# Performance work log

Hardware: AMD Instinct MI355X
Metric: run time of the kernel (lower is better)

## Reference

```python
import jax, jax.numpy as jnp
import numpy as np

SEQ_LEN = 2048

def setup_inputs() -> dict:
    key = jax.random.key(0)
    k1, k2, k3 = jax.random.split(key, 3)
    B, H, S, D = 4, 16, SEQ_LEN, 64
    keys_t = jax.random.normal(k1, (B, H, S, D), dtype=jnp.float32)
    queries = jax.random.normal(k2, (B, H, S, D), dtype=jnp.float32)
    values = jax.random.normal(k3, (B, H, S, D), dtype=jnp.float32)
    return {"keys": keys_t, "queries": queries, "values": values, "head_dim": D}

def reference(keys, queries, values, head_dim):
    # scores: [B, H, S, S] = Q K^T / sqrt(d)
    scale = 1.0 / jnp.sqrt(jnp.float32(head_dim))
    scores = jnp.einsum('bhqd,bhkd->bhqk', queries, keys) * scale
    S = scores.shape[-1]
    # causal mask: positions where tril == 0 (k > q) get -inf
    causal = jnp.tril(jnp.ones((S, S), dtype=bool))
    scores = jnp.where(causal, scores, -jnp.inf)
    attn = jax.nn.softmax(scores, axis=-1)
    # dropout p=0.0 -> identity
    return jnp.einsum('bhqk,bhkd->bhqd', attn, values)
```

## Files before the change

kernel.cpp:

```cpp
#include <hip/hip_runtime.h>
#include <hip/hip_bf16.h>

typedef __bf16 bf16x8 __attribute__((ext_vector_type(8)));
typedef __bf16 bf16x4 __attribute__((ext_vector_type(4)));
typedef float  f32x4  __attribute__((ext_vector_type(4)));

#define S_LEN 2048
#define DH    64
#define QB    64
#define KVB   64
#define NT    (S_LEN / KVB)
#define TILE_ELEMS 8192
#define TILE_BYTES 16384
#define L2E   1.44269504088896f

__device__ __forceinline__ int swz(int row, int col) {
    return (row << 6) + ((((col >> 3) ^ row) & 7) << 3) + (col & 7);
}

__device__ __forceinline__ void gl2lds16(const void* g, void* l) {
    __builtin_amdgcn_global_load_lds(
        (const __attribute__((address_space(1))) void*)g,
        (__attribute__((address_space(3))) void*)l, 16, 0, 0);
}

__device__ __forceinline__ float fexp2(float x) {
    return __builtin_amdgcn_exp2f(x);
}

__launch_bounds__(256, 4)
__global__ void prep_kv(const float* __restrict__ Kg,
                        const float* __restrict__ Vg,
                        __bf16* __restrict__ blob) {
    __shared__ __bf16 Vtmp[64 * 72];
    const int bt  = blockIdx.x;
    const int tid = threadIdx.x;
    const size_t gbase = (size_t)bt * (KVB * DH);
    const float* Kt = Kg + gbase;
    const float* Vt = Vg + gbase;
    __bf16* outK = blob + (size_t)bt * TILE_ELEMS;
    __bf16* outV = outK + 4096;

    #pragma unroll
    for (int u = 0; u < 2; ++u) {
        const int m   = tid * 2 + u;
        const int row = m >> 3, cc = m & 7;
        const int c   = cc ^ (row & 7);
        const float* src = Kt + row * DH + c * 8;
        f32x4 a = *(const f32x4*)src;
        f32x4 b = *(const f32x4*)(src + 4);
        bf16x8 o;
        #pragma unroll
        for (int j = 0; j < 4; ++j) { o[j] = (__bf16)a[j]; o[j + 4] = (__bf16)b[j]; }
        *(bf16x8*)&outK[m * 8] = o;
    }
    {
        const int kv = tid >> 2, dq = (tid & 3) * 16;
        const float* src = Vt + kv * DH + dq;
        f32x4 v0 = *(const f32x4*)src,        v1 = *(const f32x4*)(src + 4);
        f32x4 v2 = *(const f32x4*)(src + 8),  v3 = *(const f32x4*)(src + 12);
        bf16x8 o0, o1;
        #pragma unroll
        for (int j = 0; j < 4; ++j) {
            o0[j] = (__bf16)v0[j]; o0[j + 4] = (__bf16)v1[j];
            o1[j] = (__bf16)v2[j]; o1[j + 4] = (__bf16)v3[j];
        }
        *(bf16x8*)&Vtmp[kv * 72 + dq]     = o0;
        *(bf16x8*)&Vtmp[kv * 72 + dq + 8] = o1;
    }
    __syncthreads();
    #pragma unroll
    for (int u = 0; u < 2; ++u) {
        const int m  = tid * 2 + u;
        const int d  = m >> 3, cc = m & 7;
        const int S8 = cc ^ (d & 7);
        const int kc = S8 >> 2, hs = S8 & 3;
        bf16x8 o;
        #pragma unroll
        for (int j = 0; j < 8; ++j) {
            const int kv = (kc * 2 + (j >> 2)) * 16 + hs * 4 + (j & 3);
            o[j] = Vtmp[kv * 72 + d];
        }
        *(bf16x8*)&outV[m * 8] = o;
    }
}

__launch_bounds__(256, 4)
__global__ void attn_seq(const float* __restrict__ Qg,
                         float* __restrict__ Og,
                         const __bf16* __restrict__ blob) {
    __shared__ __bf16 Klds[2][4096];
    __shared__ __bf16 Vlds[2][4096];

    const int f   = blockIdx.x;
    const int chn = gridDim.x >> 3;
    const int fs  = (f & 7) * chn + (f >> 3);
    const int bh  = fs >> 4;
    const int p   = fs & 15;
    const int qa  = p;
    const int qbg = NT - 1 - p;

    const int tid = threadIdx.x;
    const int w   = tid >> 6;
    const int l   = tid & 63;
    const int lo  = l & 15;
    const int hi  = l >> 4;

    const size_t base = (size_t)bh * S_LEN * DH;
    const float* Qb = Qg + base;
    float*       Ob = Og + base;
    const char*  blobB = (const char*)(blob + (size_t)bh * NT * TILE_ELEMS);

    int koff[4][2];
    #pragma unroll
    for (int c = 0; c < 4; ++c) {
        koff[c][0] = swz(c * 16 + lo, hi * 8);
        koff[c][1] = swz(c * 16 + lo, 32 + hi * 8);
    }

    bf16x8 bq0, bq1, bqB0, bqB1;
    {
        const float* pa = Qb + (size_t)(qa  * QB + w * 16 + lo) * DH + hi * 8;
        const float* pb = Qb + (size_t)(qbg * QB + w * 16 + lo) * DH + hi * 8;
        f32x4 a0 = *(const f32x4*)pa,        a1 = *(const f32x4*)(pa + 4);
        f32x4 a2 = *(const f32x4*)(pa + 32), a3 = *(const f32x4*)(pa + 36);
        f32x4 b0 = *(const f32x4*)pb,        b1 = *(const f32x4*)(pb + 4);
        f32x4 b2 = *(const f32x4*)(pb + 32), b3 = *(const f32x4*)(pb + 36);
        #pragma unroll
        for (int j = 0; j < 4; ++j) {
            bq0[j]  = (__bf16)(a0[j] * 0.125f); bq0[j + 4]  = (__bf16)(a1[j] * 0.125f);
            bq1[j]  = (__bf16)(a2[j] * 0.125f); bq1[j + 4]  = (__bf16)(a3[j] * 0.125f);
            bqB0[j] = (__bf16)(b0[j] * 0.125f); bqB0[j + 4] = (__bf16)(b1[j] * 0.125f);
            bqB1[j] = (__bf16)(b2[j] * 0.125f); bqB1[j + 4] = (__bf16)(b3[j] * 0.125f);
        }
    }

    f32x4 oacc[4];
    #pragma unroll
    for (int n = 0; n < 4; ++n) oacc[n] = (f32x4){0.f, 0.f, 0.f, 0.f};
    float mrow = -1e30f, lrow = 0.f;

    auto stage = [&](int buf, int t) {
        const char* tb = blobB + (size_t)t * TILE_BYTES;
        char* kd = (char*)&Klds[buf][w * 1024];
        char* vd = (char*)&Vlds[buf][w * 1024];
        const char* ks = tb + w * 2048 + l * 16;
        const char* vs = tb + 8192 + w * 2048 + l * 16;
        gl2lds16(ks,        kd);
        gl2lds16(ks + 1024, kd + 1024);
        gl2lds16(vs,        vd);
        gl2lds16(vs + 1024, vd + 1024);
    };

    auto writeO = [&](int qt) {
        const float linv = 1.0f / lrow;
        const int   q    = qt * QB + w * 16 + lo;
        #pragma unroll
        for (int n = 0; n < 4; ++n) {
            f32x4 o;
            #pragma unroll
            for (int r = 0; r < 4; ++r) o[r] = oacc[n][r] * linv;
            *(f32x4*)(Ob + (size_t)q * DH + n * 16 + hi * 4) = o;
        }
    };

    stage(0, 0);
    __syncthreads();

    for (int u = 0; u <= 32; ++u) {
        const int cur = u & 1;
        if (u < 32) {
            const int tn = (u + 1 <= qa) ? (u + 1) : (u - qa);
            stage(cur ^ 1, tn);
        }
        const bool diag = (u == qa) || (u == 32);
        const __bf16* Kc = &Klds[cur][0];
        const __bf16* Vc = &Vlds[cur][0];

        f32x4 sc[4];
        __builtin_amdgcn_s_setprio(1);
        #pragma unroll
        for (int c = 0; c < 4; ++c) {
            bf16x8 ak0 = *(const bf16x8*)&Kc[koff[c][0]];
            bf16x8 ak1 = *(const bf16x8*)&Kc[koff[c][1]];
            f32x4 acc = (f32x4){0.f, 0.f, 0.f, 0.f};
            acc = __builtin_amdgcn_mfma_f32_16x16x32_bf16(ak0, bq0, acc, 0, 0, 0);
            acc = __builtin_amdgcn_mfma_f32_16x16x32_bf16(ak1, bq1, acc, 0, 0, 0);
            sc[c] = acc;
        }
        __builtin_amdgcn_s_setprio(0);

        if (diag) {
            const int qloc = w * 16 + lo;
            #pragma unroll
            for (int c = 0; c < 4; ++c)
                #pragma unroll
                for (int r = 0; r < 4; ++r)
                    if (c * 16 + hi * 4 + r > qloc) sc[c][r] = -1e30f;
        }

        float pm = -1e30f;
        #pragma unroll
        for (int c = 0; c < 4; ++c)
            pm = fmaxf(pm, fmaxf(fmaxf(sc[c][0], sc[c][1]),
                                 fmaxf(sc[c][2], sc[c][3])));
        pm = fmaxf(pm, __shfl_xor(pm, 16, 64));
        pm = fmaxf(pm, __shfl_xor(pm, 32, 64));

        if (!__all(pm - mrow <= 5.545f)) {
            const float mn = fmaxf(mrow, pm);
            const float fr = fexp2((mrow - mn) * L2E);
            mrow = mn; lrow *= fr;
            #pragma unroll
            for (int n = 0; n < 4; ++n) oacc[n] *= fr;
        }
        const float mL = mrow * L2E;
        float rs = 0.f;
        #pragma unroll
        for (int c = 0; c < 4; ++c)
            #pragma unroll
            for (int r = 0; r < 4; ++r) {
                float pe = fexp2(fmaf(sc[c][r], L2E, -mL));
                sc[c][r] = pe;
                rs += pe;
            }
        rs += __shfl_xor(rs, 16, 64);
        rs += __shfl_xor(rs, 32, 64);
        lrow += rs;

        bf16x8 pb[2];
        #pragma unroll
        for (int kc = 0; kc < 2; ++kc)
            #pragma unroll
            for (int j = 0; j < 8; ++j)
                pb[kc][j] = (__bf16)sc[kc * 2 + (j >> 2)][j & 3];

        __builtin_amdgcn_s_setprio(1);
        #pragma unroll
        for (int n = 0; n < 4; ++n) {
            bf16x8 av0 = *(const bf16x8*)&Vc[koff[n][0]];
            bf16x8 av1 = *(const bf16x8*)&Vc[koff[n][1]];
            oacc[n] = __builtin_amdgcn_mfma_f32_16x16x32_bf16(av0, pb[0], oacc[n], 0, 0, 0);
            oacc[n] = __builtin_amdgcn_mfma_f32_16x16x32_bf16(av1, pb[1], oacc[n], 0, 0, 0);
        }
        __builtin_amdgcn_s_setprio(0);

        __syncthreads();

        if (u == qa) {
            writeO(qa);
            #pragma unroll
            for (int n = 0; n < 4; ++n) oacc[n] = (f32x4){0.f, 0.f, 0.f, 0.f};
            mrow = -1e30f; lrow = 0.f;
            bq0 = bqB0; bq1 = bqB1;
        }
    }

    writeO(qbg);
}

__launch_bounds__(256, 4)
__global__ void attn_fwd(const float* __restrict__ Kg,
                         const float* __restrict__ Qg,
                         const float* __restrict__ Vg,
                         float* __restrict__ Og) {
    __shared__ __bf16 Klds[64 * 64];
    __shared__ __bf16 Vlds[64 * 64];

    const int qb  = blockIdx.x;
    const int bh  = blockIdx.y;
    const int tid = threadIdx.x;
    const int w   = tid >> 6;
    const int l   = tid & 63;
    const int lo  = l & 15;
    const int hi  = l >> 4;

    const int    q0   = qb * QB;
    const size_t base = (size_t)bh * S_LEN * DH;
    const float* Kb = Kg + base;
    const float* Qb = Qg + base;
    const float* Vb = Vg + base;
    float*       Ob = Og + base;

    bf16x8 bq[2];
    {
        const int qrow = q0 + w * 16 + lo;
        #pragma unroll
        for (int dc = 0; dc < 2; ++dc) {
            const float* p = Qb + (size_t)qrow * DH + dc * 32 + hi * 8;
            f32x4 v0 = *(const f32x4*)p;
            f32x4 v1 = *(const f32x4*)(p + 4);
            #pragma unroll
            for (int j = 0; j < 4; ++j) {
                bq[dc][j]     = (__bf16)(v0[j] * 0.125f);
                bq[dc][j + 4] = (__bf16)(v1[j] * 0.125f);
            }
        }
    }

    f32x4 oacc[4];
    #pragma unroll
    for (int n = 0; n < 4; ++n) oacc[n] = (f32x4){0.f, 0.f, 0.f, 0.f};
    float mrow = -1e30f, lrow = 0.f;

    const int krr = tid >> 4;
    const int kc4 = (tid & 15) * 4;

    for (int t = 0; t <= qb; ++t) {
        const int kv0 = t * KVB;
        {
            const float* kp = Kb + (size_t)kv0 * DH + kc4;
            #pragma unroll
            for (int i = 0; i < 4; ++i) {
                const int row = i * 16 + krr;
                f32x4 k4 = *(const f32x4*)(kp + (size_t)row * DH);
                bf16x4 kb;
                #pragma unroll
                for (int j = 0; j < 4; ++j) kb[j] = (__bf16)k4[j];
                *(bf16x4*)&Klds[swz(row, kc4)] = kb;
            }
        }
        {
            const float* vp = Vb + (size_t)kv0 * DH + l;
            float vv[16];
            #pragma unroll
            for (int i = 0; i < 16; ++i) {
                const int s  = w * 16 + i;
                const int kc = s >> 5, hs = (s >> 3) & 3, j = s & 7;
                const int kv = (kc * 2 + (j >> 2)) * 16 + hs * 4 + (j & 3);
                vv[i] = vp[(size_t)kv * DH];
            }
            bf16x8 v0, v1;
            #pragma unroll
            for (int i = 0; i < 8; ++i) { v0[i] = (__bf16)vv[i]; v1[i] = (__bf16)vv[8 + i]; }
            *(bf16x8*)&Vlds[swz(l, w * 16)]     = v0;
            *(bf16x8*)&Vlds[swz(l, w * 16 + 8)] = v1;
        }
        __syncthreads();

        const bool diag = (t == qb);
        const int  cmax = diag ? (w + 1) : 4;
        f32x4 sc[4];
        #pragma unroll
        for (int c = 0; c < 4; ++c) {
            if (c < cmax) {
                f32x4 acc = (f32x4){0.f, 0.f, 0.f, 0.f};
                #pragma unroll
                for (int dc = 0; dc < 2; ++dc) {
                    bf16x8 ak = *(const bf16x8*)&Klds[swz(c * 16 + lo, dc * 32 + hi * 8)];
                    acc = __builtin_amdgcn_mfma_f32_16x16x32_bf16(ak, bq[dc], acc, 0, 0, 0);
                }
                sc[c] = acc;
            } else {
                sc[c] = (f32x4){-1e30f, -1e30f, -1e30f, -1e30f};
            }
        }
        if (diag) {
            #pragma unroll
            for (int r = 0; r < 4; ++r)
                if (hi * 4 + r > lo) sc[w][r] = -1e30f;
        }

        float pm = -1e30f;
        #pragma unroll
        for (int c = 0; c < 4; ++c)
            #pragma unroll
            for (int r = 0; r < 4; ++r) pm = fmaxf(pm, sc[c][r]);
        pm = fmaxf(pm, __shfl_xor(pm, 16, 64));
        pm = fmaxf(pm, __shfl_xor(pm, 32, 64));

        const float mn = fmaxf(mrow, pm);
        const float fr = __expf(mrow - mn);
        mrow = mn;
        float rs = 0.f;
        #pragma unroll
        for (int c = 0; c < 4; ++c)
            #pragma unroll
            for (int r = 0; r < 4; ++r) {
                float pe = __expf(sc[c][r] - mn);
                sc[c][r] = pe;
                rs += pe;
            }
        rs += __shfl_xor(rs, 16, 64);
        rs += __shfl_xor(rs, 32, 64);
        lrow = lrow * fr + rs;
        #pragma unroll
        for (int n = 0; n < 4; ++n) oacc[n] *= fr;

        bf16x8 pb[2];
        #pragma unroll
        for (int kc = 0; kc < 2; ++kc)
            #pragma unroll
            for (int j = 0; j < 8; ++j)
                pb[kc][j] = (__bf16)sc[kc * 2 + (j >> 2)][j & 3];

        #pragma unroll
        for (int n = 0; n < 4; ++n) {
            #pragma unroll
            for (int kc = 0; kc < 2; ++kc) {
                bf16x8 av = *(const bf16x8*)&Vlds[swz(n * 16 + lo, kc * 32 + hi * 8)];
                oacc[n] = __builtin_amdgcn_mfma_f32_16x16x32_bf16(av, pb[kc], oacc[n], 0, 0, 0);
            }
        }
        __syncthreads();
    }

    const float linv = 1.0f / lrow;
    const int   q    = q0 + w * 16 + lo;
    #pragma unroll
    for (int n = 0; n < 4; ++n) {
        f32x4 o;
        #pragma unroll
        for (int r = 0; r < 4; ++r) o[r] = oacc[n][r] * linv;
        *(f32x4*)(Ob + (size_t)q * DH + n * 16 + hi * 4) = o;
    }
}

extern "C" void kernel_launch(void* const* d_in, const int* in_sizes, int n_in,
                              void* d_out, int out_size, void* d_ws, size_t ws_size,
                              hipStream_t stream) {
    const float* keys    = (const float*)d_in[0];
    const float* queries = (const float*)d_in[1];
    const float* values  = (const float*)d_in[2];
    float* out = (float*)d_out;

    const int    BH   = in_sizes[0] / (S_LEN * DH);
    const size_t need = (size_t)BH * NT * TILE_BYTES;
    const int    nblk = (NT / 2) * BH;

    if (ws_size >= need && (nblk % 8) == 0) {
        prep_kv<<<dim3(BH * NT), 256, 0, stream>>>(keys, values, (__bf16*)d_ws);
        attn_seq<<<dim3(nblk), 256, 0, stream>>>(queries, out,
                                                 (const __bf16*)d_ws);
    } else {
        attn_fwd<<<dim3(S_LEN / QB, BH), 256, 0, stream>>>(keys, queries, values, out);
    }
}
```

Before: 83.34 us.

## Split long causal query blocks across two KV halves and merge partial outputs

Adds a new attention kernel where each 128-thread block handles a 64-row query tile with two 16-row groups per wave. Query tiles in the upper half of the sequence are split into two KV-range parts whose partial output, max and sum are written to workspace, and a separate merge kernel combines them. Lower-half tiles are processed whole. The aim is to balance causal work across blocks and give each wave more MFMA reuse of K/V fragments. It also adds a lazy rescale that skips the output rescale when the running max grows by at most a small threshold. In exchange it pays an extra kernel launch, workspace traffic for the partials, and uses half-size blocks. The old fallback kernel is removed, so nothing runs if workspace is too small.

```diff
diff --git a/kernel.cpp b/kernel.cpp
--- a/kernel.cpp
+++ b/kernel.cpp
@@ -12,6 +12,7 @@
 #define NT    (S_LEN / KVB)
 #define TILE_ELEMS 8192
 #define TILE_BYTES 16384
+#define PSLOT 4224
 #define L2E   1.44269504088896f
 
 __device__ __forceinline__ int swz(int row, int col) {
@@ -85,6 +86,239 @@
     }
 }
 
+__launch_bounds__(128, 2)
+__global__ void attn_sp(const float* __restrict__ Qg,
+                        float* __restrict__ Og,
+                        const __bf16* __restrict__ blob,
+                        float* __restrict__ partials) {
+    __shared__ __bf16 Klds[2][4096];
+    __shared__ __bf16 Vlds[2][4096];
+
+    const int bh = blockIdx.x;
+    const int j  = blockIdx.y;
+    int qb, part, t0, len;
+    if (j < 32) {
+        qb   = 31 - (j >> 1);
+        part = j & 1;
+        const int h = (qb + 2) >> 1;
+        t0  = part ? h : 0;
+        len = part ? (qb + 1 - h) : h;
+    } else {
+        qb   = 47 - j;
+        part = 2;
+        t0   = 0;
+        len  = qb + 1;
+    }
+    const bool hasDiag = (part != 0);
+    const int  diagIt  = hasDiag ? len - 1 : -1;
+
+    const int tid = threadIdx.x;
+    const int w   = tid >> 6;
+    const int l   = tid & 63;
+    const int lo  = l & 15;
+    const int hi  = l >> 4;
+
+    const size_t base = (size_t)bh * S_LEN * DH;
+    const float* Qb = Qg + base;
+    float*       Ob = Og + base;
+    const char*  blobB = (const char*)(blob + (size_t)bh * NT * TILE_ELEMS);
+
+    int koff[4][2];
+    #pragma unroll
+    for (int c = 0; c < 4; ++c) {
+        koff[c][0] = swz(c * 16 + lo, hi * 8);
+        koff[c][1] = swz(c * 16 + lo, 32 + hi * 8);
+    }
+
+    bf16x8 bq[2][2];
+    #pragma unroll
+    for (int g = 0; g < 2; ++g) {
+        const float* pq = Qb + (size_t)(qb * QB + w * 32 + g * 16 + lo) * DH + hi * 8;
+        f32x4 a0 = *(const f32x4*)pq,        a1 = *(const f32x4*)(pq + 4);
+        f32x4 a2 = *(const f32x4*)(pq + 32), a3 = *(const f32x4*)(pq + 36);
+        #pragma unroll
+        for (int jj = 0; jj < 4; ++jj) {
+            bq[g][0][jj]     = (__bf16)(a0[jj] * 0.125f);
+            bq[g][0][jj + 4] = (__bf16)(a1[jj] * 0.125f);
+            bq[g][1][jj]     = (__bf16)(a2[jj] * 0.125f);
+            bq[g][1][jj + 4] = (__bf16)(a3[jj] * 0.125f);
+        }
+    }
+
+    f32x4 oacc[2][4];
+    #pragma unroll
+    for (int g = 0; g < 2; ++g)
+        #pragma unroll
+        for (int n = 0; n < 4; ++n) oacc[g][n] = (f32x4){0.f, 0.f, 0.f, 0.f};
+    float mrow[2] = {-1e30f, -1e30f}, lrow[2] = {0.f, 0.f};
+
+    auto stage = [&](int buf, int t) {
+        const char* tb = blobB + (size_t)t * TILE_BYTES;
+        char* kd = (char*)&Klds[buf][0] + w * 4096;
+        char* vd = (char*)&Vlds[buf][0] + w * 4096;
+        const char* ks = tb + w * 4096 + l * 16;
+        const char* vs = tb + 8192 + w * 4096 + l * 16;
+        #pragma unroll
+        for (int i = 0; i < 4; ++i) {
+            gl2lds16(ks + i * 1024, kd + i * 1024);
+            gl2lds16(vs + i * 1024, vd + i * 1024);
+        }
+    };
+
+    stage(0, t0);
+    __syncthreads();
+
+    for (int it = 0; it < len; ++it) {
+        const int cur = it & 1;
+        if (it + 1 < len) stage(cur ^ 1, t0 + it + 1);
+        const bool diag = (it == diagIt);
+        const __bf16* Kc = &Klds[cur][0];
+        const __bf16* Vc = &Vlds[cur][0];
+
+        f32x4 sc[2][4];
+        __builtin_amdgcn_s_setprio(1);
+        #pragma unroll
+        for (int c = 0; c < 4; ++c) {
+            bf16x8 ak0 = *(const bf16x8*)&Kc[koff[c][0]];
+            bf16x8 ak1 = *(const bf16x8*)&Kc[koff[c][1]];
+            #pragma unroll
+            for (int g = 0; g < 2; ++g) {
+                f32x4 acc = (f32x4){0.f, 0.f, 0.f, 0.f};
+                acc = __builtin_amdgcn_mfma_f32_16x16x32_bf16(ak0, bq[g][0], acc, 0, 0, 0);
+                acc = __builtin_amdgcn_mfma_f32_16x16x32_bf16(ak1, bq[g][1], acc, 0, 0, 0);
+                sc[g][c] = acc;
+            }
+        }
+        __builtin_amdgcn_s_setprio(0);
+
+        if (diag) {
+            #pragma unroll
+            for (int g = 0; g < 2; ++g) {
+                const int qloc = w * 32 + g * 16 + lo;
+                #pragma unroll
+                for (int c = 0; c < 4; ++c)
+                    #pragma unroll
+                    for (int r = 0; r < 4; ++r)
+                        if (c * 16 + hi * 4 + r > qloc) sc[g][c][r] = -1e30f;
+            }
+        }
+
+        bf16x8 pb[2][2];
+        #pragma unroll
+        for (int g = 0; g < 2; ++g) {
+            float pm = -1e30f;
+            #pragma unroll
+            for (int c = 0; c < 4; ++c)
+                pm = fmaxf(pm, fmaxf(fmaxf(sc[g][c][0], sc[g][c][1]),
+                                     fmaxf(sc[g][c][2], sc[g][c][3])));
+            pm = fmaxf(pm, __shfl_xor(pm, 16, 64));
+            pm = fmaxf(pm, __shfl_xor(pm, 32, 64));
+            if (!__all(pm - mrow[g] <= 5.545f)) {
+                const float mn = fmaxf(mrow[g], pm);
+                const float fr = fexp2((mrow[g] - mn) * L2E);
+                mrow[g] = mn; lrow[g] *= fr;
+                #pragma unroll
+                for (int n = 0; n < 4; ++n) oacc[g][n] *= fr;
+            }
+            const float mL = mrow[g] * L2E;
+            float rs = 0.f;
+            #pragma unroll
+            for (int c = 0; c < 4; ++c)
+                #pragma unroll
+                for (int r = 0; r < 4; ++r) {
+                    float pe = fexp2(fmaf(sc[g][c][r], L2E, -mL));
+                    sc[g][c][r] = pe;
+                    rs += pe;
+                }
+            rs += __shfl_xor(rs, 16, 64);
+            rs += __shfl_xor(rs, 32, 64);
+            lrow[g] += rs;
+            #pragma unroll
+            for (int kc = 0; kc < 2; ++kc)
+                #pragma unroll
+                for (int jj = 0; jj < 8; ++jj)
+                    pb[g][kc][jj] = (__bf16)sc[g][kc * 2 + (jj >> 2)][jj & 3];
+        }
+
+        __builtin_amdgcn_s_setprio(1);
+        #pragma unroll
+        for (int n = 0; n < 4; ++n) {
+            bf16x8 av0 = *(const bf16x8*)&Vc[koff[n][0]];
+            bf16x8 av1 = *(const bf16x8*)&Vc[koff[n][1]];
+            #pragma unroll
+            for (int g = 0; g < 2; ++g) {
+                oacc[g][n] = __builtin_amdgcn_mfma_f32_16x16x32_bf16(av0, pb[g][0], oacc[g][n], 0, 0, 0);
+                oacc[g][n] = __builtin_amdgcn_mfma_f32_16x16x32_bf16(av1, pb[g][1], oacc[g][n], 0, 0, 0);
+            }
+        }
+        __builtin_amdgcn_s_setprio(0);
+
+        __syncthreads();
+    }
+
+    if (part == 2) {
+        #pragma unroll
+        for (int g = 0; g < 2; ++g) {
+            const float linv = 1.0f / lrow[g];
+            const int   q    = qb * QB + w * 32 + g * 16 + lo;
+            #pragma unroll
+            for (int n = 0; n < 4; ++n) {
+                f32x4 o;
+                #pragma unroll
+                for (int r = 0; r < 4; ++r) o[r] = oacc[g][n][r] * linv;
+                *(f32x4*)(Ob + (size_t)q * DH + n * 16 + hi * 4) = o;
+            }
+        }
+    } else {
+        const int pi = bh * 16 + (qb - 16);
+        float* fb = partials + (size_t)pi * 2 * PSLOT + part * PSLOT;
+        #pragma unroll
+        for (int g = 0; g < 2; ++g) {
+            const int row = w * 32 + g * 16 + lo;
+            #pragma unroll
+            for (int n = 0; n < 4; ++n)
+                *(f32x4*)&fb[row * 64 + n * 16 + hi * 4] = oacc[g][n];
+            if (hi == 0) {
+                fb[4096 + row] = mrow[g];
+                fb[4160 + row] = lrow[g];
+            }
+        }
+    }
+}
+
+__launch_bounds__(256, 4)
+__global__ void attn_merge(float* __restrict__ Og,
+                           const float* __restrict__ partials) {
+    const int bh = blockIdx.x;
+    const int y  = blockIdx.y;
+    const int qb = 16 + y;
+    const int pi = bh * 16 + y;
+    const float* s0 = partials + (size_t)pi * 2 * PSLOT;
+    const float* s1 = s0 + PSLOT;
+
+    const int tid = threadIdx.x;
+    const int row = tid >> 2;
+    const int cb  = (tid & 3) * 16;
+
+    const float m0 = s0[4096 + row], l0 = s0[4160 + row];
+    const float m1 = s1[4096 + row], l1 = s1[4160 + row];
+    const float M  = fmaxf(m0, m1);
+    const float w0 = fexp2((m0 - M) * L2E);
+    const float w1 = fexp2((m1 - M) * L2E);
+    const float inv = 1.0f / (w0 * l0 + w1 * l1);
+
+    float* out = Og + ((size_t)bh * S_LEN + qb * QB + row) * DH + cb;
+    #pragma unroll
+    for (int i = 0; i < 4; ++i) {
+        f32x4 a = *(const f32x4*)&s0[row * 64 + cb + i * 4];
+        f32x4 b = *(const f32x4*)&s1[row * 64 + cb + i * 4];
+        f32x4 o;
+        #pragma unroll
+        for (int r = 0; r < 4; ++r) o[r] = (w0 * a[r] + w1 * b[r]) * inv;
+        *(f32x4*)&out[i * 4] = o;
+    }
+}
+
 __launch_bounds__(256, 4)
 __global__ void attn_seq(const float* __restrict__ Qg,
                          float* __restrict__ Og,
@@ -127,11 +361,11 @@
         f32x4 b0 = *(const f32x4*)pb,        b1 = *(const f32x4*)(pb + 4);
         f32x4 b2 = *(const f32x4*)(pb + 32), b3 = *(const f32x4*)(pb + 36);
         #pragma unroll
-        for (int j = 0; j < 4; ++j) {
-            bq0[j]  = (__bf16)(a0[j] * 0.125f); bq0[j + 4]  = (__bf16)(a1[j] * 0.125f);
-            bq1[j]  = (__bf16)(a2[j] * 0.125f); bq1[j + 4]  = (__bf16)(a3[j] * 0.125f);
-            bqB0[j] = (__bf16)(b0[j] * 0.125f); bqB0[j + 4] = (__bf16)(b1[j] * 0.125f);
-            bqB1[j] = (__bf16)(b2[j] * 0.125f); bqB1[j + 4] = (__bf16)(b3[j] * 0.125f);
+        for (int jj = 0; jj < 4; ++jj) {
+            bq0[jj]  = (__bf16)(a0[jj] * 0.125f); bq0[jj + 4]  = (__bf16)(a1[jj] * 0.125f);
+            bq1[jj]  = (__bf16)(a2[jj] * 0.125f); bq1[jj + 4]  = (__bf16)(a3[jj] * 0.125f);
+            bqB0[jj] = (__bf16)(b0[jj] * 0.125f); bqB0[jj + 4] = (__bf16)(b1[jj] * 0.125f);
+            bqB1[jj] = (__bf16)(b2[jj] * 0.125f); bqB1[jj + 4] = (__bf16)(b3[jj] * 0.125f);
         }
     }
 
@@ -232,8 +466,8 @@
         #pragma unroll
         for (int kc = 0; kc < 2; ++kc)
             #pragma unroll
-            for (int j = 0; j < 8; ++j)
-                pb[kc][j] = (__bf16)sc[kc * 2 + (j >> 2)][j & 3];
+            for (int jj = 0; jj < 8; ++jj)
+                pb[kc][jj] = (__bf16)sc[kc * 2 + (jj >> 2)][jj & 3];
 
         __builtin_amdgcn_s_setprio(1);
         #pragma unroll
@@ -257,163 +491,6 @@
     }
 
     writeO(qbg);
-}
-
-__launch_bounds__(256, 4)
-__global__ void attn_fwd(const float* __restrict__ Kg,
-                         const float* __restrict__ Qg,
-                         const float* __restrict__ Vg,
-                         float* __restrict__ Og) {
-    __shared__ __bf16 Klds[64 * 64];
-    __shared__ __bf16 Vlds[64 * 64];
-
-    const int qb  = blockIdx.x;
-    const int bh  = blockIdx.y;
-    const int tid = threadIdx.x;
-    const int w   = tid >> 6;
-    const int l   = tid & 63;
-    const int lo  = l & 15;
-    const int hi  = l >> 4;
-
-    const int    q0   = qb * QB;
-    const size_t base = (size_t)bh * S_LEN * DH;
-    const float* Kb = Kg + base;
-    const float* Qb = Qg + base;
-    const float* Vb = Vg + base;
-    float*       Ob = Og + base;
-
-    bf16x8 bq[2];
-    {
-        const int qrow = q0 + w * 16 + lo;
-        #pragma unroll
-        for (int dc = 0; dc < 2; ++dc) {
-            const float* p = Qb + (size_t)qrow * DH + dc * 32 + hi * 8;
-            f32x4 v0 = *(const f32x4*)p;
-            f32x4 v1 = *(const f32x4*)(p + 4);
-            #pragma unroll
-            for (int j = 0; j < 4; ++j) {
-                bq[dc][j]     = (__bf16)(v0[j] * 0.125f);
-                bq[dc][j + 4] = (__bf16)(v1[j] * 0.125f);
-            }
-        }
-    }
-
-    f32x4 oacc[4];
-    #pragma unroll
-    for (int n = 0; n < 4; ++n) oacc[n] = (f32x4){0.f, 0.f, 0.f, 0.f};
-    float mrow = -1e30f, lrow = 0.f;
-
-    const int krr = tid >> 4;
-    const int kc4 = (tid & 15) * 4;
-
-    for (int t = 0; t <= qb; ++t) {
-        const int kv0 = t * KVB;
-        {
-            const float* kp = Kb + (size_t)kv0 * DH + kc4;
-            #pragma unroll
-            for (int i = 0; i < 4; ++i) {
-                const int row = i * 16 + krr;
-                f32x4 k4 = *(const f32x4*)(kp + (size_t)row * DH);
-                bf16x4 kb;
-                #pragma unroll
-                for (int j = 0; j < 4; ++j) kb[j] = (__bf16)k4[j];
-                *(bf16x4*)&Klds[swz(row, kc4)] = kb;
-            }
-        }
-        {
-            const float* vp = Vb + (size_t)kv0 * DH + l;
-            float vv[16];
-            #pragma unroll
-            for (int i = 0; i < 16; ++i) {
-                const int s  = w * 16 + i;
-                const int kc = s >> 5, hs = (s >> 3) & 3, j = s & 7;
-                const int kv = (kc * 2 + (j >> 2)) * 16 + hs * 4 + (j & 3);
-                vv[i] = vp[(size_t)kv * DH];
-            }
-            bf16x8 v0, v1;
-            #pragma unroll
-            for (int i = 0; i < 8; ++i) { v0[i] = (__bf16)vv[i]; v1[i] = (__bf16)vv[8 + i]; }
-            *(bf16x8*)&Vlds[swz(l, w * 16)]     = v0;
-            *(bf16x8*)&Vlds[swz(l, w * 16 + 8)] = v1;
-        }
-        __syncthreads();
-
-        const bool diag = (t == qb);
-        const int  cmax = diag ? (w + 1) : 4;
-        f32x4 sc[4];
-        #pragma unroll
-        for (int c = 0; c < 4; ++c) {
-            if (c < cmax) {
-                f32x4 acc = (f32x4){0.f, 0.f, 0.f, 0.f};
-                #pragma unroll
-                for (int dc = 0; dc < 2; ++dc) {
-                    bf16x8 ak = *(const bf16x8*)&Klds[swz(c * 16 + lo, dc * 32 + hi * 8)];
-                    acc = __builtin_amdgcn_mfma_f32_16x16x32_bf16(ak, bq[dc], acc, 0, 0, 0);
-                }
-                sc[c] = acc;
-            } else {
-                sc[c] = (f32x4){-1e30f, -1e30f, -1e30f, -1e30f};
-            }
-        }
-        if (diag) {
-            #pragma unroll
-            for (int r = 0; r < 4; ++r)
-                if (hi * 4 + r > lo) sc[w][r] = -1e30f;
-        }
-
-        float pm = -1e30f;
-        #pragma unroll
-        for (int c = 0; c < 4; ++c)
-            #pragma unroll
-            for (int r = 0; r < 4; ++r) pm = fmaxf(pm, sc[c][r]);
-        pm = fmaxf(pm, __shfl_xor(pm, 16, 64));
-        pm = fmaxf(pm, __shfl_xor(pm, 32, 64));
-
-        const float mn = fmaxf(mrow, pm);
-        const float fr = __expf(mrow - mn);
-        mrow = mn;
-        float rs = 0.f;
-        #pragma unroll
-        for (int c = 0; c < 4; ++c)
-            #pragma unroll
-            for (int r = 0; r < 4; ++r) {
-                float pe = __expf(sc[c][r] - mn);
-                sc[c][r] = pe;
-                rs += pe;
-            }
-        rs += __shfl_xor(rs, 16, 64);
-        rs += __shfl_xor(rs, 32, 64);
-        lrow = lrow * fr + rs;
-        #pragma unroll
-        for (int n = 0; n < 4; ++n) oacc[n] *= fr;
-
-        bf16x8 pb[2];
-        #pragma unroll
-        for (int kc = 0; kc < 2; ++kc)
-            #pragma unroll
-            for (int j = 0; j < 8; ++j)
-                pb[kc][j] = (__bf16)sc[kc * 2 + (j >> 2)][j & 3];
-
-        #pragma unroll
-        for (int n = 0; n < 4; ++n) {
-            #pragma unroll
-            for (int kc = 0; kc < 2; ++kc) {
-                bf16x8 av = *(const bf16x8*)&Vlds[swz(n * 16 + lo, kc * 32 + hi * 8)];
-                oacc[n] = __builtin_amdgcn_mfma_f32_16x16x32_bf16(av, pb[kc], oacc[n], 0, 0, 0);
-            }
-        }
-        __syncthreads();
-    }
-
-    const float linv = 1.0f / lrow;
-    const int   q    = q0 + w * 16 + lo;
-    #pragma unroll
-    for (int n = 0; n < 4; ++n) {
-        f32x4 o;
-        #pragma unroll
-        for (int r = 0; r < 4; ++r) o[r] = oacc[n][r] * linv;
-        *(f32x4*)(Ob + (size_t)q * DH + n * 16 + hi * 4) = o;
-    }
 }
 
 extern "C" void kernel_launch(void* const* d_in, const int* in_sizes, int n_in,
@@ -424,15 +501,20 @@
     const float* values  = (const float*)d_in[2];
     float* out = (float*)d_out;
 
-    const int    BH   = in_sizes[0] / (S_LEN * DH);
-    const size_t need = (size_t)BH * NT * TILE_BYTES;
-    const int    nblk = (NT / 2) * BH;
-
-    if (ws_size >= need && (nblk % 8) == 0) {
+    const int    BH        = in_sizes[0] / (S_LEN * DH);
+    const size_t blob_b    = (size_t)BH * NT * TILE_BYTES;
+    const size_t part_b    = (size_t)BH * 16 * 2 * PSLOT * 4;
+    const int    nblk      = (NT / 2) * BH;
+
+    if (ws_size >= blob_b + part_b && BH == 64) {
+        float* partials = (float*)((char*)d_ws + blob_b);
+        prep_kv<<<dim3(BH * NT), 256, 0, stream>>>(keys, values, (__bf16*)d_ws);
+        attn_sp<<<dim3(BH, 48), 128, 0, stream>>>(queries, out,
+                                                  (const __bf16*)d_ws, partials);
+        attn_merge<<<dim3(BH, 16), 256, 0, stream>>>(out, partials);
+    } else if (ws_size >= blob_b && (nblk % 8) == 0) {
         prep_kv<<<dim3(BH * NT), 256, 0, stream>>>(keys, values, (__bf16*)d_ws);
         attn_seq<<<dim3(nblk), 256, 0, stream>>>(queries, out,
                                                  (const __bf16*)d_ws);
-    } else {
-        attn_fwd<<<dim3(S_LEN / QB, BH), 256, 0, stream>>>(keys, queries, values, out);
-    }
-}
+    }
+}
```

Result: slower. 104.1 us (+24.9%).

## Split KV work across two blocks per query-tile pair with partial-result merge

Applied to the files above, without the earlier changes.

Adds a kernel that processes 32-row KV subtiles and splits each pair of causal query tiles across two blocks. One block does the short tile plus part of the long tile, the other does the rest, and each writes bf16 partial outputs with row max and sum. A small merge kernel combines the two partials for the upper query tiles. The aim is to double grid parallelism and balance work per block at higher occupancy, at the cost of an extra launch, partial-output traffic and bf16 rounding of the partials. The old fallback kernel is removed.

```diff
diff --git a/kernel.cpp b/kernel.cpp
--- a/kernel.cpp
+++ b/kernel.cpp
@@ -85,6 +85,239 @@
     }
 }
 
+__launch_bounds__(256, 8)
+__global__ void attn32(const float* __restrict__ Qg,
+                       float* __restrict__ Og,
+                       const __bf16* __restrict__ blob,
+                       __bf16* __restrict__ Opart,
+                       float* __restrict__ mlpart) {
+    __shared__ __bf16 Klds[2][2048];
+    __shared__ __bf16 Vlds[2][2048];
+
+    const int f   = blockIdx.x;
+    const int chn = gridDim.x >> 3;
+    const int fs  = (f & 7) * chn + (f >> 3);
+    const int bh  = fs >> 5;
+    const int r   = fs & 31;
+    const int Qp  = r >> 1;
+    const int hc  = r & 1;
+
+    const int qtA = Qp;
+    const int qtB = 31 - Qp;
+
+    const int tid = threadIdx.x;
+    const int w   = tid >> 6;
+    const int l   = tid & 63;
+    const int lo  = l & 15;
+    const int hi  = l >> 4;
+
+    const size_t base = (size_t)bh * S_LEN * DH;
+    const float* Qb = Qg + base;
+    float*       Ob = Og + base;
+    const char*  blobB = (const char*)(blob + (size_t)bh * NT * TILE_ELEMS);
+
+    const int lenA = (hc == 0) ? (2 * Qp + 2) : 0;
+    const int bOff = (hc == 0) ? -(2 * Qp + 2) : (31 - 2 * Qp);
+
+    int koff[2][2];
+    #pragma unroll
+    for (int c = 0; c < 2; ++c) {
+        koff[c][0] = swz(c * 16 + lo, hi * 8);
+        koff[c][1] = swz(c * 16 + lo, 32 + hi * 8);
+    }
+    int voff[4];
+    #pragma unroll
+    for (int n = 0; n < 4; ++n) {
+        const int d = n * 16 + lo;
+        voff[n] = d * 32 + (hi ^ ((d >> 1) & 3)) * 8;
+    }
+    const int sd = tid >> 2, su = tid & 3;
+    int vsrc[2];
+    #pragma unroll
+    for (int h = 0; h < 2; ++h) {
+        const int g = 4 * h + (su ^ ((sd >> 1) & 3));
+        vsrc[h] = 8192 + sd * 128 + ((g ^ (sd & 7)) * 16);
+    }
+
+    bf16x8 bq0, bq1;
+    auto loadQ = [&](int qt) {
+        const float* p = Qb + (size_t)(qt * QB + w * 16 + lo) * DH + hi * 8;
+        f32x4 a0 = *(const f32x4*)p,        a1 = *(const f32x4*)(p + 4);
+        f32x4 a2 = *(const f32x4*)(p + 32), a3 = *(const f32x4*)(p + 36);
+        #pragma unroll
+        for (int j = 0; j < 4; ++j) {
+            bq0[j] = (__bf16)(a0[j] * 0.125f); bq0[j + 4] = (__bf16)(a1[j] * 0.125f);
+            bq1[j] = (__bf16)(a2[j] * 0.125f); bq1[j + 4] = (__bf16)(a3[j] * 0.125f);
+        }
+    };
+    loadQ(hc == 0 ? qtA : qtB);
+
+    f32x4 oacc[4];
+    #pragma unroll
+    for (int n = 0; n < 4; ++n) oacc[n] = (f32x4){0.f, 0.f, 0.f, 0.f};
+    float mrow = -1e30f, lrow = 0.f;
+
+    auto stage = [&](int buf, int t32) {
+        const int T = t32 >> 1, h = t32 & 1;
+        const char* tb = blobB + (size_t)T * TILE_BYTES;
+        gl2lds16(tb + h * 4096 + tid * 16, (char*)&Klds[buf][0] + tid * 16);
+        gl2lds16(tb + vsrc[h],             (char*)&Vlds[buf][0] + tid * 16);
+    };
+
+    auto writeO = [&](int qt) {
+        const float linv = 1.0f / lrow;
+        const int   q    = qt * QB + w * 16 + lo;
+        #pragma unroll
+        for (int n = 0; n < 4; ++n) {
+            f32x4 o;
+            #pragma unroll
+            for (int rr = 0; rr < 4; ++rr) o[rr] = oacc[n][rr] * linv;
+            *(f32x4*)(Ob + (size_t)q * DH + n * 16 + hi * 4) = o;
+        }
+    };
+
+    stage(0, (hc == 0) ? 0 : bOff);
+    __syncthreads();
+
+    for (int it = 0; it < 33; ++it) {
+        const int  cur = it & 1;
+        const bool isA = (it < lenA);
+        const int  qt  = isA ? qtA : qtB;
+        const int  t32 = isA ? it : it + bOff;
+        if (it + 1 < 33) {
+            const int nt32 = (it + 1 < lenA) ? (it + 1) : (it + 1 + bOff);
+            stage(cur ^ 1, nt32);
+        }
+        const __bf16* Kc = &Klds[cur][0];
+        const __bf16* Vc = &Vlds[cur][0];
+
+        f32x4 sc[2];
+        __builtin_amdgcn_s_setprio(1);
+        #pragma unroll
+        for (int c = 0; c < 2; ++c) {
+            bf16x8 ak0 = *(const bf16x8*)&Kc[koff[c][0]];
+            bf16x8 ak1 = *(const bf16x8*)&Kc[koff[c][1]];
+            f32x4 acc = (f32x4){0.f, 0.f, 0.f, 0.f};
+            acc = __builtin_amdgcn_mfma_f32_16x16x32_bf16(ak0, bq0, acc, 0, 0, 0);
+            acc = __builtin_amdgcn_mfma_f32_16x16x32_bf16(ak1, bq1, acc, 0, 0, 0);
+            sc[c] = acc;
+        }
+        __builtin_amdgcn_s_setprio(0);
+
+        if (t32 >= 2 * qt) {
+            const int qg = qt * 64 + w * 16 + lo;
+            #pragma unroll
+            for (int c = 0; c < 2; ++c)
+                #pragma unroll
+                for (int rr = 0; rr < 4; ++rr)
+                    if (t32 * 32 + c * 16 + hi * 4 + rr > qg) sc[c][rr] = -1e30f;
+        }
+
+        float pm = fmaxf(fmaxf(fmaxf(sc[0][0], sc[0][1]), fmaxf(sc[0][2], sc[0][3])),
+                         fmaxf(fmaxf(sc[1][0], sc[1][1]), fmaxf(sc[1][2], sc[1][3])));
+        pm = fmaxf(pm, __shfl_xor(pm, 16, 64));
+        pm = fmaxf(pm, __shfl_xor(pm, 32, 64));
+
+        if (!__all(pm - mrow <= 5.545f)) {
+            const float mn = fmaxf(mrow, pm);
+            const float fr = fexp2((mrow - mn) * L2E);
+            mrow = mn; lrow *= fr;
+            #pragma unroll
+            for (int n = 0; n < 4; ++n) oacc[n] *= fr;
+        }
+        const float mL = mrow * L2E;
+        float rs = 0.f;
+        #pragma unroll
+        for (int c = 0; c < 2; ++c)
+            #pragma unroll
+            for (int rr = 0; rr < 4; ++rr) {
+                float pe = fexp2(fmaf(sc[c][rr], L2E, -mL));
+                sc[c][rr] = pe;
+                rs += pe;
+            }
+        rs += __shfl_xor(rs, 16, 64);
+        rs += __shfl_xor(rs, 32, 64);
+        lrow += rs;
+
+        bf16x8 pb;
+        #pragma unroll
+        for (int j = 0; j < 8; ++j)
+            pb[j] = (__bf16)sc[j >> 2][j & 3];
+
+        __builtin_amdgcn_s_setprio(1);
+        #pragma unroll
+        for (int n = 0; n < 4; ++n) {
+            bf16x8 av = *(const bf16x8*)&Vc[voff[n]];
+            oacc[n] = __builtin_amdgcn_mfma_f32_16x16x32_bf16(av, pb, oacc[n], 0, 0, 0);
+        }
+        __builtin_amdgcn_s_setprio(0);
+
+        __syncthreads();
+
+        if (hc == 0 && it == lenA - 1) {
+            writeO(qtA);
+            #pragma unroll
+            for (int n = 0; n < 4; ++n) oacc[n] = (f32x4){0.f, 0.f, 0.f, 0.f};
+            mrow = -1e30f; lrow = 0.f;
+            loadQ(qtB);
+        }
+    }
+
+    const int pidx = bh * 16 + (15 - Qp);
+    __bf16* op = Opart + ((size_t)pidx * 2 + hc) * 4096;
+    const int qloc = w * 16 + lo;
+    #pragma unroll
+    for (int n = 0; n < 4; ++n) {
+        bf16x4 ob;
+        #pragma unroll
+        for (int rr = 0; rr < 4; ++rr) ob[rr] = (__bf16)oacc[n][rr];
+        *(bf16x4*)&op[qloc * 64 + n * 16 + hi * 4] = ob;
+    }
+    if (hi == 0) {
+        float* mp = mlpart + ((size_t)pidx * 2 + hc) * 128;
+        mp[qloc]      = mrow;
+        mp[64 + qloc] = lrow;
+    }
+}
+
+__launch_bounds__(128, 8)
+__global__ void attn_merge2(float* __restrict__ Og,
+                            const __bf16* __restrict__ Opart,
+                            const float* __restrict__ mlpart) {
+    const int u  = blockIdx.x;
+    const int bh = u >> 4;
+    const int qt = 16 + (u & 15);
+    const int tid = threadIdx.x;
+    const int q  = tid >> 1;
+    const int dh = tid & 1;
+
+    const float* ml0 = mlpart + (size_t)u * 2 * 128;
+    const float* ml1 = ml0 + 128;
+    const float m0 = ml0[q], l0 = ml0[64 + q];
+    const float m1 = ml1[q], l1 = ml1[64 + q];
+    const float M  = fmaxf(m0, m1);
+    const float w0 = fexp2((m0 - M) * L2E);
+    const float w1 = fexp2((m1 - M) * L2E);
+    const float inv = 1.0f / (w0 * l0 + w1 * l1);
+
+    const __bf16* o0 = Opart + (size_t)u * 2 * 4096 + q * 64 + dh * 32;
+    const __bf16* o1 = o0 + 4096;
+    float* out = Og + ((size_t)bh * S_LEN + qt * 64 + q) * DH + dh * 32;
+    #pragma unroll
+    for (int i = 0; i < 4; ++i) {
+        bf16x8 a = *(const bf16x8*)&o0[i * 8];
+        bf16x8 b = *(const bf16x8*)&o1[i * 8];
+        f32x4 lo4, hi4;
+        #pragma unroll
+        for (int rr = 0; rr < 4; ++rr) {
+            lo4[rr] = (w0 * (float)a[rr]     + w1 * (float)b[rr])     * inv;
+            hi4[rr] = (w0 * (float)a[rr + 4] + w1 * (float)b[rr + 4]) * inv;
+        }
+        *(f32x4*)&out[i * 8]     = lo4;
+        *(f32x4*)&out[i * 8 + 4] = hi4;
+    }
+}
+
 __launch_bounds__(256, 4)
 __global__ void attn_seq(const float* __restrict__ Qg,
                          float* __restrict__ Og,
@@ -127,11 +360,11 @@
         f32x4 b0 = *(const f32x4*)pb,        b1 = *(const f32x4*)(pb + 4);
         f32x4 b2 = *(const f32x4*)(pb + 32), b3 = *(const f32x4*)(pb + 36);
         #pragma unroll
-        for (int j = 0; j < 4; ++j) {
-            bq0[j]  = (__bf16)(a0[j] * 0.125f); bq0[j + 4]  = (__bf16)(a1[j] * 0.125f);
-            bq1[j]  = (__bf16)(a2[j] * 0.125f); bq1[j + 4]  = (__bf16)(a3[j] * 0.125f);
-            bqB0[j] = (__bf16)(b0[j] * 0.125f); bqB0[j + 4] = (__bf16)(b1[j] * 0.125f);
-            bqB1[j] = (__bf16)(b2[j] * 0.125f); bqB1[j + 4] = (__bf16)(b3[j] * 0.125f);
+        for (int jj = 0; jj < 4; ++jj) {
+            bq0[jj]  = (__bf16)(a0[jj] * 0.125f); bq0[jj + 4]  = (__bf16)(a1[jj] * 0.125f);
+            bq1[jj]  = (__bf16)(a2[jj] * 0.125f); bq1[jj + 4]  = (__bf16)(a3[jj] * 0.125f);
+            bqB0[jj] = (__bf16)(b0[jj] * 0.125f); bqB0[jj + 4] = (__bf16)(b1[jj] * 0.125f);
+            bqB1[jj] = (__bf16)(b2[jj] * 0.125f); bqB1[jj + 4] = (__bf16)(b3[jj] * 0.125f);
         }
     }
 
@@ -159,7 +392,7 @@
         for (int n = 0; n < 4; ++n) {
             f32x4 o;
             #pragma unroll
-            for (int r = 0; r < 4; ++r) o[r] = oacc[n][r] * linv;
+            for (int rr = 0; rr < 4; ++rr) o[rr] = oacc[n][rr] * linv;
             *(f32x4*)(Ob + (size_t)q * DH + n * 16 + hi * 4) = o;
         }
     };
@@ -195,8 +428,8 @@
             #pragma unroll
             for (int c = 0; c < 4; ++c)
                 #pragma unroll
-                for (int r = 0; r < 4; ++r)
-                    if (c * 16 + hi * 4 + r > qloc) sc[c][r] = -1e30f;
+                for (int rr = 0; rr < 4; ++rr)
+                    if (c * 16 + hi * 4 + rr > qloc) sc[c][rr] = -1e30f;
         }
 
         float pm = -1e30f;
@@ -219,9 +452,9 @@
         #pragma unroll
         for (int c = 0; c < 4; ++c)
             #pragma unroll
-            for (int r = 0; r < 4; ++r) {
-                float pe = fexp2(fmaf(sc[c][r], L2E, -mL));
-                sc[c][r] = pe;
+            for (int rr = 0; rr < 4; ++rr) {
+                float pe = fexp2(fmaf(sc[c][rr], L2E, -mL));
+                sc[c][rr] = pe;
                 rs += pe;
             }
         rs += __shfl_xor(rs, 16, 64);
@@ -232,8 +465,8 @@
         #pragma unroll
         for (int kc = 0; kc < 2; ++kc)
             #pragma unroll
-            for (int j = 0; j < 8; ++j)
-                pb[kc][j] = (__bf16)sc[kc * 2 + (j >> 2)][j & 3];
+            for (int jj = 0; jj < 8; ++jj)
+                pb[kc][jj] = (__bf16)sc[kc * 2 + (jj >> 2)][jj & 3];
 
         __builtin_amdgcn_s_setprio(1);
         #pragma unroll
@@ -257,163 +490,6 @@
     }
 
     writeO(qbg);
-}
-
-__launch_bounds__(256, 4)
-__global__ void attn_fwd(const float* __restrict__ Kg,
-                         const float* __restrict__ Qg,
-                         const float* __restrict__ Vg,
-                         float* __restrict__ Og) {
-    __shared__ __bf16 Klds[64 * 64];
-    __shared__ __bf16 Vlds[64 * 64];
-
-    const int qb  = blockIdx.x;
-    const int bh  = blockIdx.y;
-    const int tid = threadIdx.x;
-    const int w   = tid >> 6;
-    const int l   = tid & 63;
-    const int lo  = l & 15;
-    const int hi  = l >> 4;
-
-    const int    q0   = qb * QB;
-    const size_t base = (size_t)bh * S_LEN * DH;
-    const float* Kb = Kg + base;
-    const float* Qb = Qg + base;
-    const float* Vb = Vg + base;
-    float*       Ob = Og + base;
-
-    bf16x8 bq[2];
-    {
-        const int qrow = q0 + w * 16 + lo;
-        #pragma unroll
-        for (int dc = 0; dc < 2; ++dc) {
-            const float* p = Qb + (size_t)qrow * DH + dc * 32 + hi * 8;
-            f32x4 v0 = *(const f32x4*)p;
-            f32x4 v1 = *(const f32x4*)(p + 4);
-            #pragma unroll
-            for (int j = 0; j < 4; ++j) {
-                bq[dc][j]     = (__bf16)(v0[j] * 0.125f);
-                bq[dc][j + 4] = (__bf16)(v1[j] * 0.125f);
-            }
-        }
-    }
-
-    f32x4 oacc[4];
-    #pragma unroll
-    for (int n = 0; n < 4; ++n) oacc[n] = (f32x4){0.f, 0.f, 0.f, 0.f};
-    float mrow = -1e30f, lrow = 0.f;
-
-    const int krr = tid >> 4;
-    const int kc4 = (tid & 15) * 4;
-
-    for (int t = 0; t <= qb; ++t) {
-        const int kv0 = t * KVB;
-        {
-            const float* kp = Kb + (size_t)kv0 * DH + kc4;
-            #pragma unroll
-            for (int i = 0; i < 4; ++i) {
-                const int row = i * 16 + krr;
-                f32x4 k4 = *(const f32x4*)(kp + (size_t)row * DH);
-                bf16x4 kb;
-                #pragma unroll
-                for (int j = 0; j < 4; ++j) kb[j] = (__bf16)k4[j];
-                *(bf16x4*)&Klds[swz(row, kc4)] = kb;
-            }
-        }
-        {
-            const float* vp = Vb + (size_t)kv0 * DH + l;
-            float vv[16];
-            #pragma unroll
-            for (int i = 0; i < 16; ++i) {
-                const int s  = w * 16 + i;
-                const int kc = s >> 5, hs = (s >> 3) & 3, j = s & 7;
-                const int kv = (kc * 2 + (j >> 2)) * 16 + hs * 4 + (j & 3);
-                vv[i] = vp[(size_t)kv * DH];
-            }
-            bf16x8 v0, v1;
-            #pragma unroll
-            for (int i = 0; i < 8; ++i) { v0[i] = (__bf16)vv[i]; v1[i] = (__bf16)vv[8 + i]; }
-            *(bf16x8*)&Vlds[swz(l, w * 16)]     = v0;
-            *(bf16x8*)&Vlds[swz(l, w * 16 + 8)] = v1;
-        }
-        __syncthreads();
-
-        const bool diag = (t == qb);
-        const int  cmax = diag ? (w + 1) : 4;
-        f32x4 sc[4];
-        #pragma unroll
-        for (int c = 0; c < 4; ++c) {
-            if (c < cmax) {
-                f32x4 acc = (f32x4){0.f, 0.f, 0.f, 0.f};
-                #pragma unroll
-                for (int dc = 0; dc < 2; ++dc) {
-                    bf16x8 ak = *(const bf16x8*)&Klds[swz(c * 16 + lo, dc * 32 + hi * 8)];
-                    acc = __builtin_amdgcn_mfma_f32_16x16x32_bf16(ak, bq[dc], acc, 0, 0, 0);
-                }
-                sc[c] = acc;
-            } else {
-                sc[c] = (f32x4){-1e30f, -1e30f, -1e30f, -1e30f};
-            }
-        }
-        if (diag) {
-            #pragma unroll
-            for (int r = 0; r < 4; ++r)
-                if (hi * 4 + r > lo) sc[w][r] = -1e30f;
-        }
-
-        float pm = -1e30f;
-        #pragma unroll
-        for (int c = 0; c < 4; ++c)
-            #pragma unroll
-            for (int r = 0; r < 4; ++r) pm = fmaxf(pm, sc[c][r]);
-        pm = fmaxf(pm, __shfl_xor(pm, 16, 64));
-        pm = fmaxf(pm, __shfl_xor(pm, 32, 64));
-
-        const float mn = fmaxf(mrow, pm);
-        const float fr = __expf(mrow - mn);
-        mrow = mn;
-        float rs = 0.f;
-        #pragma unroll
-        for (int c = 0; c < 4; ++c)
-            #pragma unroll
-            for (int r = 0; r < 4; ++r) {
-                float pe = __expf(sc[c][r] - mn);
-                sc[c][r] = pe;
-                rs += pe;
-            }
-        rs += __shfl_xor(rs, 16, 64);
-        rs += __shfl_xor(rs, 32, 64);
-        lrow = lrow * fr + rs;
-        #pragma unroll
-        for (int n = 0; n < 4; ++n) oacc[n] *= fr;
-
-        bf16x8 pb[2];
-        #pragma unroll
-        for (int kc = 0; kc < 2; ++kc)
-            #pragma unroll
-            for (int j = 0; j < 8; ++j)
-                pb[kc][j] = (__bf16)sc[kc * 2 + (j >> 2)][j & 3];
-
-        #pragma unroll
-        for (int n = 0; n < 4; ++n) {
-            #pragma unroll
-            for (int kc = 0; kc < 2; ++kc) {
-                bf16x8 av = *(const bf16x8*)&Vlds[swz(n * 16 + lo, kc * 32 + hi * 8)];
-                oacc[n] = __builtin_amdgcn_mfma_f32_16x16x32_bf16(av, pb[kc], oacc[n], 0, 0, 0);
-            }
-        }
-        __syncthreads();
-    }
-
-    const float linv = 1.0f / lrow;
-    const int   q    = q0 + w * 16 + lo;
-    #pragma unroll
-    for (int n = 0; n < 4; ++n) {
-        f32x4 o;
-        #pragma unroll
-        for (int r = 0; r < 4; ++r) o[r] = oacc[n][r] * linv;
-        *(f32x4*)(Ob + (size_t)q * DH + n * 16 + hi * 4) = o;
-    }
 }
 
 extern "C" void kernel_launch(void* const* d_in, const int* in_sizes, int n_in,
@@ -424,15 +500,23 @@
     const float* values  = (const float*)d_in[2];
     float* out = (float*)d_out;
 
-    const int    BH   = in_sizes[0] / (S_LEN * DH);
-    const size_t need = (size_t)BH * NT * TILE_BYTES;
-    const int    nblk = (NT / 2) * BH;
-
-    if (ws_size >= need && (nblk % 8) == 0) {
+    const int    BH     = in_sizes[0] / (S_LEN * DH);
+    const size_t blob_b = (size_t)BH * NT * TILE_BYTES;
+    const size_t op_b   = (size_t)BH * 16 * 2 * 4096 * 2;
+    const size_t ml_b   = (size_t)BH * 16 * 2 * 128 * 4;
+    const int    nblk2  = BH * 32;
+    const int    nblk1  = (NT / 2) * BH;
+
+    if (ws_size >= blob_b + op_b + ml_b && (nblk2 % 8) == 0) {
+        __bf16* blob  = (__bf16*)d_ws;
+        __bf16* Opart = (__bf16*)((char*)d_ws + blob_b);
+        float*  mlp   = (float*)((char*)d_ws + blob_b + op_b);
+        prep_kv<<<dim3(BH * NT), 256, 0, stream>>>(keys, values, blob);
+        attn32<<<dim3(nblk2), 256, 0, stream>>>(queries, out, blob, Opart, mlp);
+        attn_merge2<<<dim3(BH * 16), 128, 0, stream>>>(out, Opart, mlp);
+    } else if (ws_size >= blob_b && (nblk1 % 8) == 0) {
         prep_kv<<<dim3(BH * NT), 256, 0, stream>>>(keys, values, (__bf16*)d_ws);
-        attn_seq<<<dim3(nblk), 256, 0, stream>>>(queries, out,
-                                                 (const __bf16*)d_ws);
-    } else {
-        attn_fwd<<<dim3(S_LEN / QB, BH), 256, 0, stream>>>(keys, queries, values, out);
-    }
-}
+        attn_seq<<<dim3(nblk1), 256, 0, stream>>>(queries, out,
+                                                  (const __bf16*)d_ws);
+    }
+}
```

Result: slower. 100.8 us (+20.9%).
